# Optimization experiments

Hardware: AMD Instinct MI355X
Metric: run time of the kernel (lower is better)

Reference implementation:

```python
import jax, jax.numpy as jnp
import numpy as np

B, S = 256, 512
NQ = 1000           # n_skills
MEM, DK, DV, FC = 20, 50, 200, 50  # memory_size, key dim, value dim, final fc dim


def _kaiming(key, shape, fan_in):
    return jax.random.normal(key, shape) * np.float32(np.sqrt(2.0 / fan_in))


def setup_inputs() -> dict:
    key = jax.random.key(0)
    ks = jax.random.split(key, 12)
    q_data = jax.random.randint(ks[0], (B, S), 0, NQ + 1)
    qa_data = jax.random.randint(ks[1], (B, S), 0, 2 * NQ + 1)
    u = jax.random.uniform(ks[2], (B * S,))
    # target: -1 = masked/padding, else binary label (matches target.ge(0) masking)
    target = jnp.where(u < 0.1, -1.0, (u > 0.55).astype(jnp.float32))
    q_embed_w = _kaiming(ks[3], (NQ + 1, DK), DK)
    qa_embed_w = _kaiming(ks[4], (2 * NQ + 1, DV), DV)
    memory_key = _kaiming(ks[5], (MEM, DK), DK)
    init_memory_value = _kaiming(ks[6], (MEM, DV), DV)
    erase_w = _kaiming(ks[7], (DV, DV), DV)
    erase_b = jnp.zeros((DV,), jnp.float32)
    add_w = _kaiming(ks[8], (DV, DV), DV)
    add_b = jnp.zeros((DV,), jnp.float32)
    read_w = _kaiming(ks[9], (DV + FC, FC), DV + FC)
    read_b = jnp.zeros((FC,), jnp.float32)
    pred_w = _kaiming(ks[10], (FC, 1), FC)
    pred_b = jnp.zeros((1,), jnp.float32)
    return dict(q_data=q_data, qa_data=qa_data, target=target,
                q_embed_w=q_embed_w, qa_embed_w=qa_embed_w,
                memory_key=memory_key, init_memory_value=init_memory_value,
                erase_w=erase_w, erase_b=erase_b, add_w=add_w, add_b=add_b,
                read_w=read_w, read_b=read_b, pred_w=pred_w, pred_b=pred_b)


def reference(q_data, qa_data, target, q_embed_w, qa_embed_w, memory_key,
              init_memory_value, erase_w, erase_b, add_w, add_b,
              read_w, read_b, pred_w, pred_b):
    b = q_data.shape[0]
    q_e = q_embed_w[q_data]     # [B,S,DK]
    qa_e = qa_embed_w[qa_data]  # [B,S,DV]
    Mv0 = jnp.broadcast_to(init_memory_value, (b, MEM, DV))

    def step(Mv, xs):
        q_t, qa_t = xs                                        # [B,DK], [B,DV]
        corr = jax.nn.softmax(q_t @ memory_key.T, axis=1)     # [B,MEM] addressing
        read = jnp.einsum('bm,bmd->bd', corr, Mv)             # weighted read
        erase = jax.nn.sigmoid(qa_t @ erase_w + erase_b)      # [B,DV]
        add = jnp.tanh(qa_t @ add_w + add_b)                  # [B,DV]
        w = corr[:, :, None]                                  # [B,MEM,1]
        Mv = Mv * (1.0 - w * erase[:, None, :]) + w * add[:, None, :]
        return Mv, read

    _, reads = jax.lax.scan(step, Mv0, (q_e.transpose(1, 0, 2), qa_e.transpose(1, 0, 2)))
    reads = reads.transpose(1, 0, 2)                          # [B,S,DV]
    x = jnp.concatenate([reads, q_e], axis=-1)                # [B,S,DV+FC]
    h = jnp.tanh(x @ read_w + read_b)                         # [B,S,FC]
    logits = (h @ pred_w + pred_b).reshape(-1)                # [B*S]
    mask = target >= 0.0
    t = jnp.where(mask, target, 0.0)
    # numerically-stable BCE-with-logits, masked mean
    bce = jnp.maximum(logits, 0.0) - logits * t + jnp.log1p(jnp.exp(-jnp.abs(logits)))
    loss = jnp.sum(jnp.where(mask, bce, 0.0)) / jnp.maximum(mask.sum(), 1)
    return loss, jax.nn.sigmoid(logits)
```

## Files before the change

### kernel.cpp

```cpp
#include <hip/hip_runtime.h>
#include <math.h>

#define B_   256
#define S_   512
#define NQ_  1000
#define MEM_ 20
#define DK_  50
#define DV_  200
#define FC_  50
#define RPB  4
#define CHK  16
#define CLEN (S_/CHK)
#define NKS  7
#define XS_STRIDE 232
#define NB_EA    ((2*NQ_+1+RPB-1)/RPB)
#define NB_CORR  4
#define NB_WPACK 7
#define NB_HQ    251
#define PREP_BLOCKS (NB_EA+NB_CORR+NB_WPACK+NB_HQ)
#define MM_BLOCKS (B_*CHK)
#define SCANA_BLOCKS (B_*(CHK-1))

typedef __attribute__((ext_vector_type(8))) short bf16x8_t;
typedef __attribute__((ext_vector_type(4))) float f32x4_t;
typedef __attribute__((ext_vector_type(2))) float f32x2_t;

static __device__ __forceinline__ f32x2_t pkfma(f32x2_t a, f32x2_t b, f32x2_t c){
  return __builtin_elementwise_fma(a, b, c);
}

static __device__ __forceinline__ unsigned short f2bf(float f){
  unsigned u = __float_as_uint(f);
  unsigned r = u + 0x7fffu + ((u >> 16) & 1u);
  return (unsigned short)(r >> 16);
}
static __device__ __forceinline__ float bf2f_lo(unsigned v){ return __uint_as_float(v << 16); }
static __device__ __forceinline__ float bf2f_hi(unsigned v){ return __uint_as_float(v & 0xffff0000u); }
static __device__ __forceinline__ float ftanh(float x){
  float e = __expf(2.f*x);
  return 1.f - 2.f*__builtin_amdgcn_rcpf(e+1.f);
}
static __device__ __forceinline__ float fsigm(float x){
  return __builtin_amdgcn_rcpf(1.f+__expf(-x));
}

__global__ __launch_bounds__(256) void k_prep(
    const float* __restrict__ qaw,
    const float* __restrict__ ew, const float* __restrict__ eb,
    const float* __restrict__ aw, const float* __restrict__ ab,
    float2* __restrict__ eaTab,
    const float* __restrict__ qw, const float* __restrict__ mk,
    float* __restrict__ corrTab,
    const float* __restrict__ rw, const float* __restrict__ rb,
    const float* __restrict__ pw,
    unsigned short* __restrict__ WpFrag, float* __restrict__ pwPad,
    float* __restrict__ hq){
  __shared__ float qa[RPB*DV_];
  int blk = blockIdx.x;
  if(blk < NB_EA){
    int row0 = blk*RPB;
    for(int i=threadIdx.x; i<RPB*DV_; i+=256){
      int r = i/DV_, cc = i - r*DV_;
      int row = row0 + r;
      qa[i] = (row <= 2*NQ_) ? qaw[row*DV_+cc] : 0.f;
    }
    __syncthreads();
    int d = threadIdx.x;
    if(d >= DV_) return;
    float accE[RPB], accA[RPB];
    #pragma unroll
    for(int r=0;r<RPB;++r){ accE[r] = eb[d]; accA[r] = ab[d]; }
    float we0 = ew[d], wa0 = aw[d];
    for(int j=0;j<DV_;++j){
      int jn = (j+1 < DV_) ? j+1 : j;
      float we1 = ew[jn*DV_+d];
      float wa1 = aw[jn*DV_+d];
      #pragma unroll
      for(int r=0;r<RPB;++r){
        float x = qa[r*DV_+j];
        accE[r] = fmaf(x, we0, accE[r]);
        accA[r] = fmaf(x, wa0, accA[r]);
      }
      we0 = we1; wa0 = wa1;
    }
    #pragma unroll
    for(int r=0;r<RPB;++r){
      int row = row0 + r;
      if(row <= 2*NQ_)
        eaTab[(size_t)row*DV_+d] = make_float2(fsigm(accE[r]), ftanh(accA[r]));
    }
  } else if(blk < NB_EA+NB_CORR){
    int q = (blk-NB_EA)*256 + threadIdx.x;
    if(q > NQ_) return;
    float qv[DK_];
    #pragma unroll
    for(int j=0;j<DK_;++j) qv[j] = qw[q*DK_+j];
    float s[MEM_]; float mx = -1e30f;
    #pragma unroll
    for(int m=0;m<MEM_;++m){
      float acc = 0.f;
      #pragma unroll
      for(int j=0;j<DK_;++j) acc = fmaf(qv[j], mk[m*DK_+j], acc);
      s[m] = acc; mx = fmaxf(mx, acc);
    }
    float sum = 0.f;
    #pragma unroll
    for(int m=0;m<MEM_;++m){ s[m] = __expf(s[m]-mx); sum += s[m]; }
    float inv = __builtin_amdgcn_rcpf(sum);
    #pragma unroll
    for(int m=0;m<MEM_;++m) corrTab[q*MEM_+m] = s[m]*inv;
  } else if(blk < NB_EA+NB_CORR+NB_WPACK){
    int ks = blk - (NB_EA+NB_CORR);
    int nt = threadIdx.x >> 6;
    int lane = threadIdx.x & 63;
    int quad = lane >> 4, col = lane & 15;
    int n = nt*16 + col;
    unsigned short tmp[8];
    #pragma unroll
    for(int j=0;j<8;++j){
      int k = ks*32 + quad*8 + j;
      tmp[j] = (k < DV_ && n < FC_) ? f2bf(rw[k*FC_+n]) : (unsigned short)0;
    }
    uint4* dst = reinterpret_cast<uint4*>(WpFrag + ((size_t)(ks*4+nt)*64 + lane)*8);
    *dst = *reinterpret_cast<const uint4*>(tmp);
    if(ks == 0 && threadIdx.x < 64)
      pwPad[threadIdx.x] = (threadIdx.x < FC_) ? pw[threadIdx.x] : 0.f;
  } else {
    int idx = (blk-(NB_EA+NB_CORR+NB_WPACK))*256 + threadIdx.x;
    int q = idx >> 6, n = idx & 63;
    if(q > NQ_) return;
    float v = 0.f;
    if(n < FC_){
      float acc = rb[n];
      #pragma unroll
      for(int j=0;j<DK_;++j)
        acc = fmaf(qw[q*DK_+j], rw[(DV_+j)*FC_+n], acc);
      v = acc;
    }
    hq[q*64+n] = v;
  }
}

__global__ __launch_bounds__(256,8) void k_scanA(const int* __restrict__ qd,
    const int* __restrict__ qad,
    const float4* __restrict__ corr4,
    const float2* __restrict__ eaTab,
    unsigned* __restrict__ ABu){
  const int blk = blockIdx.x;
  const int b = blk / (CHK-1), c = blk % (CHK-1);
  const int d = threadIdx.x;
  const int dc = (d < DV_) ? d : DV_-1;
  const bool act = (d < DV_);
  const int* __restrict__ qp  = qd  + b*S_ + c*CLEN;
  const int* __restrict__ qap = qad + b*S_ + c*CLEN;

  f32x2_t A2[MEM_/2], B2[MEM_/2];
  #pragma unroll
  for(int i=0;i<MEM_/2;++i){ A2[i] = (f32x2_t){1.f,1.f}; B2[i] = (f32x2_t){0.f,0.f}; }

  int q2  = qp[1];
  int qa2 = qap[1];
  int q1s = __builtin_amdgcn_readfirstlane(qp[0]);
  int qa1 = qap[0];
  const float4* cb0 = corr4 + q1s*5;
  float4 c0 = cb0[0], c1 = cb0[1], c2 = cb0[2], c3 = cb0[3], c4 = cb0[4];
  float2 ea = eaTab[(size_t)qa1*DV_ + dc];

  #pragma unroll 2
  for(int t=0;t<CLEN;++t){
    int t2 = (t+2 < CLEN) ? t+2 : CLEN-1;
    int q3 = qp[t2], qa3 = qap[t2];
    int qs = __builtin_amdgcn_readfirstlane(q2);
    const float4* cb = corr4 + qs*5;
    float4 n0 = cb[0], n1 = cb[1], n2 = cb[2], n3 = cb[3], n4 = cb[4];
    float2 ean = eaTab[(size_t)qa2*DV_ + dc];

    const f32x2_t e2 = {ea.x, ea.x}, a2 = {ea.y, ea.y}, one2 = {1.f, 1.f};
    #define UPDA(cx, cy, i) { \
      f32x2_t cp = {cx, cy}; \
      f32x2_t al = pkfma(-cp, e2, one2); \
      f32x2_t be = cp*a2; \
      A2[i] = A2[i]*al; \
      B2[i] = pkfma(al, B2[i], be); }
    UPDA(c0.x, c0.y, 0)  UPDA(c0.z, c0.w, 1)
    UPDA(c1.x, c1.y, 2)  UPDA(c1.z, c1.w, 3)
    UPDA(c2.x, c2.y, 4)  UPDA(c2.z, c2.w, 5)
    UPDA(c3.x, c3.y, 6)  UPDA(c3.z, c3.w, 7)
    UPDA(c4.x, c4.y, 8)  UPDA(c4.z, c4.w, 9)
    #undef UPDA

    c0=n0; c1=n1; c2=n2; c3=n3; c4=n4; ea=ean;
    q2=q3; qa2=qa3;
  }
  if(act){
    unsigned* base = ABu + ((size_t)(b*(CHK-1) + c)*MEM_)*DV_ + d;
    #pragma unroll
    for(int i=0;i<MEM_/2;++i){
      base[(size_t)(2*i)*DV_]   = (unsigned)f2bf(A2[i][0]) | ((unsigned)f2bf(B2[i][0]) << 16);
      base[(size_t)(2*i+1)*DV_] = (unsigned)f2bf(A2[i][1]) | ((unsigned)f2bf(B2[i][1]) << 16);
    }
  }
}

__global__ __launch_bounds__(256) void k_prefix(const float* __restrict__ mv0,
    const unsigned* __restrict__ ABu, unsigned short* __restrict__ Mv0s){
  int i = blockIdx.x*256 + threadIdx.x;
  if(i >= B_*MEM_*DV_) return;
  int d = i % DV_;
  int m = (i / DV_) % MEM_;
  int b = i / (DV_*MEM_);
  unsigned abv[CHK-1];
  #pragma unroll
  for(int c=0;c<CHK-1;++c)
    abv[c] = ABu[((size_t)(b*(CHK-1) + c)*MEM_ + m)*DV_ + d];
  float Mv = mv0[m*DV_+d];
  #pragma unroll
  for(int c=0;c<CHK;++c){
    Mv0s[((size_t)(b*CHK + c)*MEM_ + m)*DV_ + d] = f2bf(Mv);
    if(c < CHK-1) Mv = fmaf(bf2f_lo(abv[c]), Mv, bf2f_hi(abv[c]));
  }
}

__global__ __launch_bounds__(256,8) void k_scan_mm(const int* __restrict__ qd,
    const int* __restrict__ qad,
    const float4* __restrict__ corr4,
    const float2* __restrict__ eaTab,
    const unsigned short* __restrict__ Mv0s,
    const unsigned short* __restrict__ WpFrag,
    const float* __restrict__ hq,
    const float* __restrict__ pwPad, const float* __restrict__ pb,
    const float* __restrict__ target,
    float* __restrict__ out, float2* __restrict__ partials){
  __shared__ unsigned short Xs[CLEN*XS_STRIDE];
  __shared__ float sred[2][2][16];
  __shared__ float sbce[4];

  const int blk = blockIdx.x;
  const int b = blk >> 4, c = blk & (CHK-1);
  const int d = threadIdx.x;
  const int dc = (d < DV_) ? d : DV_-1;
  const bool act = (d < DV_);
  const bool padw = (d < 224);
  const int* __restrict__ qp  = qd  + b*S_ + c*CLEN;
  const int* __restrict__ qap = qad + b*S_ + c*CLEN;

  f32x2_t Mv2[MEM_/2];
  {
    const unsigned short* base = Mv0s + ((size_t)(b*CHK + c)*MEM_)*DV_ + dc;
    #pragma unroll
    for(int i=0;i<MEM_/2;++i)
      Mv2[i] = (f32x2_t){ bf2f_lo((unsigned)base[(size_t)(2*i)*DV_]),
                          bf2f_lo((unsigned)base[(size_t)(2*i+1)*DV_]) };
  }

  int q2  = qp[1];
  int qa2 = qap[1];
  int q1s = __builtin_amdgcn_readfirstlane(qp[0]);
  int qa1 = qap[0];
  const float4* cbi = corr4 + q1s*5;
  float4 c0 = cbi[0], c1 = cbi[1], c2 = cbi[2], c3 = cbi[3], c4 = cbi[4];
  float2 ea = eaTab[(size_t)qa1*DV_ + dc];

  #pragma unroll 2
  for(int t=0;t<CLEN;++t){
    int t2 = (t+2 < CLEN) ? t+2 : CLEN-1;
    int q3 = qp[t2], qa3 = qap[t2];
    int qs = __builtin_amdgcn_readfirstlane(q2);
    const float4* cb = corr4 + qs*5;
    float4 n0 = cb[0], n1 = cb[1], n2 = cb[2], n3 = cb[3], n4 = cb[4];
    float2 ean = eaTab[(size_t)qa2*DV_ + dc];

    const f32x2_t e2 = {ea.x, ea.x}, a2 = {ea.y, ea.y};
    f32x2_t rd2 = {0.f, 0.f};
    #define UPD2(cx, cy, i) { \
      f32x2_t cp = {cx, cy}; \
      rd2 = pkfma(cp, Mv2[i], rd2); \
      Mv2[i] = pkfma(cp, pkfma(-Mv2[i], e2, a2), Mv2[i]); }
    UPD2(c0.x, c0.y, 0)  UPD2(c0.z, c0.w, 1)
    UPD2(c1.x, c1.y, 2)  UPD2(c1.z, c1.w, 3)
    UPD2(c2.x, c2.y, 4)  UPD2(c2.z, c2.w, 5)
    UPD2(c3.x, c3.y, 6)  UPD2(c3.z, c3.w, 7)
    UPD2(c4.x, c4.y, 8)  UPD2(c4.z, c4.w, 9)
    #undef UPD2

    if(padw) Xs[t*XS_STRIDE + d] = act ? f2bf(rd2[0]+rd2[1]) : (unsigned short)0;

    c0=n0; c1=n1; c2=n2; c3=n3; c4=n4; ea=ean;
    q2=q3; qa2=qa3;
  }
  __syncthreads();

  const int wave = threadIdx.x >> 6;
  const int lane = threadIdx.x & 63;
  const int col  = lane & 15, quad = lane >> 4;
  const int rt   = wave & 1;
  const int nh   = wave >> 1;
  const int mbase = rt*16;

  f32x4_t acc[2];
  acc[0] = (f32x4_t){0.f,0.f,0.f,0.f};
  acc[1] = (f32x4_t){0.f,0.f,0.f,0.f};

  #pragma unroll
  for(int ks=0;ks<NKS;++ks){
    bf16x8_t a = *reinterpret_cast<const bf16x8_t*>(Xs + (mbase+col)*XS_STRIDE + quad*8 + ks*32);
    #pragma unroll
    for(int j=0;j<2;++j){
      int nt = nh*2 + j;
      bf16x8_t bfr = *reinterpret_cast<const bf16x8_t*>(WpFrag + ((size_t)(ks*4+nt)*64 + lane)*8);
      acc[j] = __builtin_amdgcn_mfma_f32_16x16x32_bf16(a, bfr, acc[j], 0, 0, 0);
    }
  }

  float part[4];
  #pragma unroll
  for(int reg=0;reg<4;++reg){
    int mloc = mbase + quad*4 + reg;
    int q = qp[mloc];
    float s = 0.f;
    #pragma unroll
    for(int j=0;j<2;++j){
      int n = (nh*2+j)*16 + col;
      float h = acc[j][reg] + hq[q*64 + n];
      s = fmaf(pwPad[n], ftanh(h), s);
    }
    part[reg] = s;
  }
  #pragma unroll
  for(int off=1; off<16; off<<=1){
    #pragma unroll
    for(int reg=0;reg<4;++reg) part[reg] += __shfl_xor(part[reg], off, 64);
  }
  if(col == 0){
    #pragma unroll
    for(int reg=0;reg<4;++reg) sred[rt][nh][quad*4+reg] = part[reg];
  }
  __syncthreads();

  float bce = 0.f, cnt = 0.f;
  if(nh == 0 && col == 0){
    float pbv = pb[0];
    #pragma unroll
    for(int reg=0;reg<4;++reg){
      int idx = quad*4 + reg;
      int mloc = mbase + idx;
      int row = b*S_ + c*CLEN + mloc;
      float logit = sred[rt][0][idx] + sred[rt][1][idx] + pbv;
      out[1+row] = fsigm(logit);
      float t = target[row];
      if(t >= 0.f){
        cnt += 1.f;
        bce += fmaxf(logit,0.f) - logit*t + log1pf(__expf(-fabsf(logit)));
      }
    }
  }
  bce += __shfl_xor(bce, 16, 64); cnt += __shfl_xor(cnt, 16, 64);
  bce += __shfl_xor(bce, 32, 64); cnt += __shfl_xor(cnt, 32, 64);
  if(lane == 0 && nh == 0){ sbce[wave] = bce; sbce[2+wave] = cnt; }
  __syncthreads();
  if(threadIdx.x == 0)
    partials[blk] = make_float2(sbce[0]+sbce[1], sbce[2]+sbce[3]);
}

__global__ __launch_bounds__(256) void k_fin(const float2* __restrict__ partials,
                                             float* __restrict__ out){
  float bce = 0.f, cnt = 0.f;
  for(int i=threadIdx.x; i<MM_BLOCKS; i+=256){
    float2 p = partials[i];
    bce += p.x; cnt += p.y;
  }
  #pragma unroll
  for(int off=32; off>0; off>>=1){
    bce += __shfl_down(bce, off, 64);
    cnt += __shfl_down(cnt, off, 64);
  }
  __shared__ float sb[4], sc[4];
  int w = threadIdx.x >> 6;
  if((threadIdx.x & 63) == 0){ sb[w] = bce; sc[w] = cnt; }
  __syncthreads();
  if(threadIdx.x == 0){
    float Bt = sb[0]+sb[1]+sb[2]+sb[3];
    float Ct = sc[0]+sc[1]+sc[2]+sc[3];
    out[0] = Bt / fmaxf(Ct, 1.f);
  }
}

extern "C" void kernel_launch(void* const* d_in, const int* in_sizes, int n_in,
                              void* d_out, int out_size, void* d_ws, size_t ws_size,
                              hipStream_t stream){
  const int*   qd     = (const int*)d_in[0];
  const int*   qad    = (const int*)d_in[1];
  const float* target = (const float*)d_in[2];
  const float* qw     = (const float*)d_in[3];
  const float* qaw    = (const float*)d_in[4];
  const float* mk     = (const float*)d_in[5];
  const float* mv0    = (const float*)d_in[6];
  const float* ew     = (const float*)d_in[7];
  const float* eb     = (const float*)d_in[8];
  const float* aw     = (const float*)d_in[9];
  const float* ab     = (const float*)d_in[10];
  const float* rw     = (const float*)d_in[11];
  const float* rb     = (const float*)d_in[12];
  const float* pw     = (const float*)d_in[13];
  const float* pb     = (const float*)d_in[14];
  float* out = (float*)d_out;

  char* ws = (char*)d_ws;
  size_t off = 0;
  float2* partials = (float2*)(ws + off);            off += (size_t)MM_BLOCKS*8;
  float* corrTab  = (float*)(ws + off);              off += (((size_t)(NQ_+1)*MEM_*4 + 255)/256)*256;
  float2* eaTab   = (float2*)(ws + off);             off += (((size_t)(2*NQ_+1)*DV_*8 + 255)/256)*256;
  unsigned* ABu   = (unsigned*)(ws + off);           off += (size_t)SCANA_BLOCKS*MEM_*DV_*4;
  unsigned short* Mv0s = (unsigned short*)(ws + off); off += (size_t)MM_BLOCKS*MEM_*DV_*2;
  unsigned short* WpFrag = (unsigned short*)(ws + off); off += ((size_t)NKS*4*64*8*2 + 255)/256*256;
  float* pwPad    = (float*)(ws + off);              off += 256;
  float* hq       = (float*)(ws + off);              off += (size_t)(NQ_+1)*64*4;

  k_prep<<<dim3(PREP_BLOCKS), dim3(256), 0, stream>>>(qaw, ew, eb, aw, ab, eaTab,
                                                      qw, mk, corrTab,
                                                      rw, rb, pw, WpFrag, pwPad, hq);
  k_scanA<<<dim3(SCANA_BLOCKS), dim3(256), 0, stream>>>(qd, qad, (const float4*)corrTab, (const float2*)eaTab, ABu);
  k_prefix<<<dim3((B_*MEM_*DV_+255)/256), dim3(256), 0, stream>>>(mv0, ABu, Mv0s);
  k_scan_mm<<<dim3(MM_BLOCKS), dim3(256), 0, stream>>>(qd, qad, (const float4*)corrTab, (const float2*)eaTab,
                                                       Mv0s, WpFrag, hq, pwPad, pb, target, out, partials);
  k_fin<<<dim3(1), dim3(256), 0, stream>>>(partials, out);
}
```

Measured before the change: 226.9 us.

## Halve scan chunk count and process each chunk in two 32-step sub-tiles

Reduces the number of sequence chunks per batch row from 16 to 8, so each scan block walks 64 steps in two 32-step sub-tiles, running the MFMA readout and BCE after each sub-tile from a reused shared buffer. This halves the chunk-prefix work and the Mv0 state traffic (fewer chunk starting states to compute and load), and halves the block count. In exchange each block's sequential scan is twice as long, there are fewer blocks to hide latency, and an extra barrier pair is added per sub-tile. It relies on the prep kernels using CHK consistently for the chunk-start states.

```diff
diff --git a/kernel.cpp b/kernel.cpp
--- a/kernel.cpp
+++ b/kernel.cpp
@@ -9,8 +9,9 @@
 #define DV_  200
 #define FC_  50
 #define RPB  4
-#define CHK  16
+#define CHK  8
 #define CLEN (S_/CHK)
+#define SUB  32
 #define NKS  7
 #define XS_STRIDE 232
 #define NB_EA    ((2*NQ_+1+RPB-1)/RPB)
@@ -231,12 +232,12 @@
     const float* __restrict__ pwPad, const float* __restrict__ pb,
     const float* __restrict__ target,
     float* __restrict__ out, float2* __restrict__ partials){
-  __shared__ unsigned short Xs[CLEN*XS_STRIDE];
+  __shared__ unsigned short Xs[SUB*XS_STRIDE];
   __shared__ float sred[2][2][16];
   __shared__ float sbce[4];
 
   const int blk = blockIdx.x;
-  const int b = blk >> 4, c = blk & (CHK-1);
+  const int b = blk >> 3, c = blk & (CHK-1);
   const int d = threadIdx.x;
   const int dc = (d < DV_) ? d : DV_-1;
   const bool act = (d < DV_);
@@ -261,35 +262,6 @@
   float4 c0 = cbi[0], c1 = cbi[1], c2 = cbi[2], c3 = cbi[3], c4 = cbi[4];
   float2 ea = eaTab[(size_t)qa1*DV_ + dc];
 
-  #pragma unroll 2
-  for(int t=0;t<CLEN;++t){
-    int t2 = (t+2 < CLEN) ? t+2 : CLEN-1;
-    int q3 = qp[t2], qa3 = qap[t2];
-    int qs = __builtin_amdgcn_readfirstlane(q2);
-    const float4* cb = corr4 + qs*5;
-    float4 n0 = cb[0], n1 = cb[1], n2 = cb[2], n3 = cb[3], n4 = cb[4];
-    float2 ean = eaTab[(size_t)qa2*DV_ + dc];
-
-    const f32x2_t e2 = {ea.x, ea.x}, a2 = {ea.y, ea.y};
-    f32x2_t rd2 = {0.f, 0.f};
-    #define UPD2(cx, cy, i) { \
-      f32x2_t cp = {cx, cy}; \
-      rd2 = pkfma(cp, Mv2[i], rd2); \
-      Mv2[i] = pkfma(cp, pkfma(-Mv2[i], e2, a2), Mv2[i]); }
-    UPD2(c0.x, c0.y, 0)  UPD2(c0.z, c0.w, 1)
-    UPD2(c1.x, c1.y, 2)  UPD2(c1.z, c1.w, 3)
-    UPD2(c2.x, c2.y, 4)  UPD2(c2.z, c2.w, 5)
-    UPD2(c3.x, c3.y, 6)  UPD2(c3.z, c3.w, 7)
-    UPD2(c4.x, c4.y, 8)  UPD2(c4.z, c4.w, 9)
-    #undef UPD2
-
-    if(padw) Xs[t*XS_STRIDE + d] = act ? f2bf(rd2[0]+rd2[1]) : (unsigned short)0;
-
-    c0=n0; c1=n1; c2=n2; c3=n3; c4=n4; ea=ean;
-    q2=q3; qa2=qa3;
-  }
-  __syncthreads();
-
   const int wave = threadIdx.x >> 6;
   const int lane = threadIdx.x & 63;
   const int col  = lane & 15, quad = lane >> 4;
@@ -297,63 +269,99 @@
   const int nh   = wave >> 1;
   const int mbase = rt*16;
 
-  f32x4_t acc[2];
-  acc[0] = (f32x4_t){0.f,0.f,0.f,0.f};
-  acc[1] = (f32x4_t){0.f,0.f,0.f,0.f};
+  float bceAcc = 0.f, cntAcc = 0.f;
+  const float pbv = pb[0];
 
   #pragma unroll
-  for(int ks=0;ks<NKS;++ks){
-    bf16x8_t a = *reinterpret_cast<const bf16x8_t*>(Xs + (mbase+col)*XS_STRIDE + quad*8 + ks*32);
-    #pragma unroll
-    for(int j=0;j<2;++j){
-      int nt = nh*2 + j;
-      bf16x8_t bfr = *reinterpret_cast<const bf16x8_t*>(WpFrag + ((size_t)(ks*4+nt)*64 + lane)*8);
-      acc[j] = __builtin_amdgcn_mfma_f32_16x16x32_bf16(a, bfr, acc[j], 0, 0, 0);
-    }
-  }
-
-  float part[4];
-  #pragma unroll
-  for(int reg=0;reg<4;++reg){
-    int mloc = mbase + quad*4 + reg;
-    int q = qp[mloc];
-    float s = 0.f;
-    #pragma unroll
-    for(int j=0;j<2;++j){
-      int n = (nh*2+j)*16 + col;
-      float h = acc[j][reg] + hq[q*64 + n];
-      s = fmaf(pwPad[n], ftanh(h), s);
-    }
-    part[reg] = s;
-  }
-  #pragma unroll
-  for(int off=1; off<16; off<<=1){
-    #pragma unroll
-    for(int reg=0;reg<4;++reg) part[reg] += __shfl_xor(part[reg], off, 64);
-  }
-  if(col == 0){
-    #pragma unroll
-    for(int reg=0;reg<4;++reg) sred[rt][nh][quad*4+reg] = part[reg];
-  }
-  __syncthreads();
-
-  float bce = 0.f, cnt = 0.f;
-  if(nh == 0 && col == 0){
-    float pbv = pb[0];
+  for(int sub=0; sub<2; ++sub){
+    #pragma unroll 2
+    for(int i=0;i<SUB;++i){
+      int t = sub*SUB + i;
+      int t2 = (t+2 < CLEN) ? t+2 : CLEN-1;
+      int q3 = qp[t2], qa3 = qap[t2];
+      int qs = __builtin_amdgcn_readfirstlane(q2);
+      const float4* cb = corr4 + qs*5;
+      float4 n0 = cb[0], n1 = cb[1], n2 = cb[2], n3 = cb[3], n4 = cb[4];
+      float2 ean = eaTab[(size_t)qa2*DV_ + dc];
+
+      const f32x2_t e2 = {ea.x, ea.x}, a2 = {ea.y, ea.y};
+      f32x2_t rd2 = {0.f, 0.f};
+      #define UPD2(cx, cy, i2) { \
+        f32x2_t cp = {cx, cy}; \
+        rd2 = pkfma(cp, Mv2[i2], rd2); \
+        Mv2[i2] = pkfma(cp, pkfma(-Mv2[i2], e2, a2), Mv2[i2]); }
+      UPD2(c0.x, c0.y, 0)  UPD2(c0.z, c0.w, 1)
+      UPD2(c1.x, c1.y, 2)  UPD2(c1.z, c1.w, 3)
+      UPD2(c2.x, c2.y, 4)  UPD2(c2.z, c2.w, 5)
+      UPD2(c3.x, c3.y, 6)  UPD2(c3.z, c3.w, 7)
+      UPD2(c4.x, c4.y, 8)  UPD2(c4.z, c4.w, 9)
+      #undef UPD2
+
+      if(padw) Xs[i*XS_STRIDE + d] = act ? f2bf(rd2[0]+rd2[1]) : (unsigned short)0;
+
+      c0=n0; c1=n1; c2=n2; c3=n3; c4=n4; ea=ean;
+      q2=q3; qa2=qa3;
+    }
+    __syncthreads();
+
+    f32x4_t acc[2];
+    acc[0] = (f32x4_t){0.f,0.f,0.f,0.f};
+    acc[1] = (f32x4_t){0.f,0.f,0.f,0.f};
+
+    #pragma unroll
+    for(int ks=0;ks<NKS;++ks){
+      bf16x8_t a = *reinterpret_cast<const bf16x8_t*>(Xs + (mbase+col)*XS_STRIDE + quad*8 + ks*32);
+      #pragma unroll
+      for(int j=0;j<2;++j){
+        int nt = nh*2 + j;
+        bf16x8_t bfr = *reinterpret_cast<const bf16x8_t*>(WpFrag + ((size_t)(ks*4+nt)*64 + lane)*8);
+        acc[j] = __builtin_amdgcn_mfma_f32_16x16x32_bf16(a, bfr, acc[j], 0, 0, 0);
+      }
+    }
+
+    float part[4];
     #pragma unroll
     for(int reg=0;reg<4;++reg){
-      int idx = quad*4 + reg;
-      int mloc = mbase + idx;
-      int row = b*S_ + c*CLEN + mloc;
-      float logit = sred[rt][0][idx] + sred[rt][1][idx] + pbv;
-      out[1+row] = fsigm(logit);
-      float t = target[row];
-      if(t >= 0.f){
-        cnt += 1.f;
-        bce += fmaxf(logit,0.f) - logit*t + log1pf(__expf(-fabsf(logit)));
+      int mloc = mbase + quad*4 + reg;
+      int q = qp[sub*SUB + mloc];
+      float s = 0.f;
+      #pragma unroll
+      for(int j=0;j<2;++j){
+        int n = (nh*2+j)*16 + col;
+        float h = acc[j][reg] + hq[q*64 + n];
+        s = fmaf(pwPad[n], ftanh(h), s);
       }
-    }
-  }
+      part[reg] = s;
+    }
+    #pragma unroll
+    for(int off=1; off<16; off<<=1){
+      #pragma unroll
+      for(int reg=0;reg<4;++reg) part[reg] += __shfl_xor(part[reg], off, 64);
+    }
+    if(col == 0){
+      #pragma unroll
+      for(int reg=0;reg<4;++reg) sred[rt][nh][quad*4+reg] = part[reg];
+    }
+    __syncthreads();
+
+    if(nh == 0 && col == 0){
+      #pragma unroll
+      for(int reg=0;reg<4;++reg){
+        int idx = quad*4 + reg;
+        int mloc = mbase + idx;
+        int row = b*S_ + c*CLEN + sub*SUB + mloc;
+        float logit = sred[rt][0][idx] + sred[rt][1][idx] + pbv;
+        out[1+row] = fsigm(logit);
+        float t = target[row];
+        if(t >= 0.f){
+          cntAcc += 1.f;
+          bceAcc += fmaxf(logit,0.f) - logit*t + log1pf(__expf(-fabsf(logit)));
+        }
+      }
+    }
+  }
+
+  float bce = bceAcc, cnt = cntAcc;
   bce += __shfl_xor(bce, 16, 64); cnt += __shfl_xor(cnt, 16, 64);
   bce += __shfl_xor(bce, 32, 64); cnt += __shfl_xor(cnt, 32, 64);
   if(lane == 0 && nh == 0){ sbce[wave] = bce; sbce[2+wave] = cnt; }
```

New measurement: 227.6 us. About the same (+0.3%).

## Move weight packing into scanA launch, deepen eaTab prefetch, skip chunk-0 state store

Applied to the files above, without the earlier changes.

Moves the WpFrag/pwPad/hq preparation blocks out of the prep kernel into extra blocks of the scanA launch, so the prep kernel on the critical path is shorter. Deepens the erase/add table prefetch in both scan loops to two steps ahead, with index lookahead of four. Chunk 0 now reads the initial memory directly instead of a stored bf16 copy, so the prefix kernel skips that write. The hq gather indices are loaded early in scan_mm. This costs extra registers, which may reduce occupancy.

```diff
diff --git a/kernel.cpp b/kernel.cpp
--- a/kernel.cpp
+++ b/kernel.cpp
@@ -17,9 +17,10 @@
 #define NB_CORR  4
 #define NB_WPACK 7
 #define NB_HQ    251
-#define PREP_BLOCKS (NB_EA+NB_CORR+NB_WPACK+NB_HQ)
+#define PREP1_BLOCKS (NB_EA+NB_CORR)
 #define MM_BLOCKS (B_*CHK)
 #define SCANA_BLOCKS (B_*(CHK-1))
+#define SCANA_TOTAL (SCANA_BLOCKS+NB_WPACK+NB_HQ)
 
 typedef __attribute__((ext_vector_type(8))) short bf16x8_t;
 typedef __attribute__((ext_vector_type(4))) float f32x4_t;
@@ -44,17 +45,13 @@
   return __builtin_amdgcn_rcpf(1.f+__expf(-x));
 }
 
-__global__ __launch_bounds__(256) void k_prep(
+__global__ __launch_bounds__(256) void k_prep1(
     const float* __restrict__ qaw,
     const float* __restrict__ ew, const float* __restrict__ eb,
     const float* __restrict__ aw, const float* __restrict__ ab,
     float2* __restrict__ eaTab,
     const float* __restrict__ qw, const float* __restrict__ mk,
-    float* __restrict__ corrTab,
-    const float* __restrict__ rw, const float* __restrict__ rb,
-    const float* __restrict__ pw,
-    unsigned short* __restrict__ WpFrag, float* __restrict__ pwPad,
-    float* __restrict__ hq){
+    float* __restrict__ corrTab){
   __shared__ float qa[RPB*DV_];
   int blk = blockIdx.x;
   if(blk < NB_EA){
@@ -89,7 +86,7 @@
       if(row <= 2*NQ_)
         eaTab[(size_t)row*DV_+d] = make_float2(fsigm(accE[r]), ftanh(accA[r]));
     }
-  } else if(blk < NB_EA+NB_CORR){
+  } else {
     int q = (blk-NB_EA)*256 + threadIdx.x;
     if(q > NQ_) return;
     float qv[DK_];
@@ -109,35 +106,6 @@
     float inv = __builtin_amdgcn_rcpf(sum);
     #pragma unroll
     for(int m=0;m<MEM_;++m) corrTab[q*MEM_+m] = s[m]*inv;
-  } else if(blk < NB_EA+NB_CORR+NB_WPACK){
-    int ks = blk - (NB_EA+NB_CORR);
-    int nt = threadIdx.x >> 6;
-    int lane = threadIdx.x & 63;
-    int quad = lane >> 4, col = lane & 15;
-    int n = nt*16 + col;
-    unsigned short tmp[8];
-    #pragma unroll
-    for(int j=0;j<8;++j){
-      int k = ks*32 + quad*8 + j;
-      tmp[j] = (k < DV_ && n < FC_) ? f2bf(rw[k*FC_+n]) : (unsigned short)0;
-    }
-    uint4* dst = reinterpret_cast<uint4*>(WpFrag + ((size_t)(ks*4+nt)*64 + lane)*8);
-    *dst = *reinterpret_cast<const uint4*>(tmp);
-    if(ks == 0 && threadIdx.x < 64)
-      pwPad[threadIdx.x] = (threadIdx.x < FC_) ? pw[threadIdx.x] : 0.f;
-  } else {
-    int idx = (blk-(NB_EA+NB_CORR+NB_WPACK))*256 + threadIdx.x;
-    int q = idx >> 6, n = idx & 63;
-    if(q > NQ_) return;
-    float v = 0.f;
-    if(n < FC_){
-      float acc = rb[n];
-      #pragma unroll
-      for(int j=0;j<DK_;++j)
-        acc = fmaf(qw[q*DK_+j], rw[(DV_+j)*FC_+n], acc);
-      v = acc;
-    }
-    hq[q*64+n] = v;
   }
 }
 
@@ -145,8 +113,48 @@
     const int* __restrict__ qad,
     const float4* __restrict__ corr4,
     const float2* __restrict__ eaTab,
-    unsigned* __restrict__ ABu){
+    unsigned* __restrict__ ABu,
+    const float* __restrict__ qw,
+    const float* __restrict__ rw, const float* __restrict__ rb,
+    const float* __restrict__ pw,
+    unsigned short* __restrict__ WpFrag, float* __restrict__ pwPad,
+    float* __restrict__ hq){
   const int blk = blockIdx.x;
+  if(blk >= SCANA_BLOCKS){
+    int xblk = blk - SCANA_BLOCKS;
+    if(xblk < NB_WPACK){
+      int ks = xblk;
+      int nt = threadIdx.x >> 6;
+      int lane = threadIdx.x & 63;
+      int quad = lane >> 4, col = lane & 15;
+      int n = nt*16 + col;
+      unsigned short tmp[8];
+      #pragma unroll
+      for(int j=0;j<8;++j){
+        int k = ks*32 + quad*8 + j;
+        tmp[j] = (k < DV_ && n < FC_) ? f2bf(rw[k*FC_+n]) : (unsigned short)0;
+      }
+      uint4* dst = reinterpret_cast<uint4*>(WpFrag + ((size_t)(ks*4+nt)*64 + lane)*8);
+      *dst = *reinterpret_cast<const uint4*>(tmp);
+      if(ks == 0 && threadIdx.x < 64)
+        pwPad[threadIdx.x] = (threadIdx.x < FC_) ? pw[threadIdx.x] : 0.f;
+    } else {
+      int idx = (xblk-NB_WPACK)*256 + threadIdx.x;
+      int q = idx >> 6, n = idx & 63;
+      if(q > NQ_) return;
+      float v = 0.f;
+      if(n < FC_){
+        float acc = rb[n];
+        #pragma unroll
+        for(int j=0;j<DK_;++j)
+          acc = fmaf(qw[q*DK_+j], rw[(DV_+j)*FC_+n], acc);
+        v = acc;
+      }
+      hq[q*64+n] = v;
+    }
+    return;
+  }
+
   const int b = blk / (CHK-1), c = blk % (CHK-1);
   const int d = threadIdx.x;
   const int dc = (d < DV_) ? d : DV_-1;
@@ -158,22 +166,25 @@
   #pragma unroll
   for(int i=0;i<MEM_/2;++i){ A2[i] = (f32x2_t){1.f,1.f}; B2[i] = (f32x2_t){0.f,0.f}; }
 
-  int q2  = qp[1];
-  int qa2 = qap[1];
-  int q1s = __builtin_amdgcn_readfirstlane(qp[0]);
-  int qa1 = qap[0];
+  int q2   = qp[1];
+  int qaT2 = qap[2];
+  int qaT3 = qap[3];
+  int q1s  = __builtin_amdgcn_readfirstlane(qp[0]);
   const float4* cb0 = corr4 + q1s*5;
   float4 c0 = cb0[0], c1 = cb0[1], c2 = cb0[2], c3 = cb0[3], c4 = cb0[4];
-  float2 ea = eaTab[(size_t)qa1*DV_ + dc];
+  float2 ea  = eaTab[(size_t)qap[0]*DV_ + dc];
+  float2 ean = eaTab[(size_t)qap[1]*DV_ + dc];
 
   #pragma unroll 2
   for(int t=0;t<CLEN;++t){
     int t2 = (t+2 < CLEN) ? t+2 : CLEN-1;
-    int q3 = qp[t2], qa3 = qap[t2];
+    int t4 = (t+4 < CLEN) ? t+4 : CLEN-1;
+    int q3 = qp[t2];
+    int qaN = qap[t4];
     int qs = __builtin_amdgcn_readfirstlane(q2);
     const float4* cb = corr4 + qs*5;
     float4 n0 = cb[0], n1 = cb[1], n2 = cb[2], n3 = cb[3], n4 = cb[4];
-    float2 ean = eaTab[(size_t)qa2*DV_ + dc];
+    float2 eann = eaTab[(size_t)qaT2*DV_ + dc];
 
     const f32x2_t e2 = {ea.x, ea.x}, a2 = {ea.y, ea.y}, one2 = {1.f, 1.f};
     #define UPDA(cx, cy, i) { \
@@ -189,8 +200,9 @@
     UPDA(c4.x, c4.y, 8)  UPDA(c4.z, c4.w, 9)
     #undef UPDA
 
-    c0=n0; c1=n1; c2=n2; c3=n3; c4=n4; ea=ean;
-    q2=q3; qa2=qa3;
+    c0=n0; c1=n1; c2=n2; c3=n3; c4=n4;
+    ea=ean; ean=eann;
+    q2=q3; qaT2=qaT3; qaT3=qaN;
   }
   if(act){
     unsigned* base = ABu + ((size_t)(b*(CHK-1) + c)*MEM_)*DV_ + d;
@@ -215,9 +227,10 @@
     abv[c] = ABu[((size_t)(b*(CHK-1) + c)*MEM_ + m)*DV_ + d];
   float Mv = mv0[m*DV_+d];
   #pragma unroll
-  for(int c=0;c<CHK;++c){
+  for(int c=1;c<CHK;++c){
+    unsigned v = abv[c-1];
+    Mv = fmaf(bf2f_lo(v), Mv, bf2f_hi(v));
     Mv0s[((size_t)(b*CHK + c)*MEM_ + m)*DV_ + d] = f2bf(Mv);
-    if(c < CHK-1) Mv = fmaf(bf2f_lo(abv[c]), Mv, bf2f_hi(abv[c]));
   }
 }
 
@@ -225,6 +238,7 @@
     const int* __restrict__ qad,
     const float4* __restrict__ corr4,
     const float2* __restrict__ eaTab,
+    const float* __restrict__ mv0,
     const unsigned short* __restrict__ Mv0s,
     const unsigned short* __restrict__ WpFrag,
     const float* __restrict__ hq,
@@ -244,8 +258,23 @@
   const int* __restrict__ qp  = qd  + b*S_ + c*CLEN;
   const int* __restrict__ qap = qad + b*S_ + c*CLEN;
 
+  const int wave = threadIdx.x >> 6;
+  const int lane = threadIdx.x & 63;
+  const int col  = lane & 15, quad = lane >> 4;
+  const int rt   = wave & 1;
+  const int nh   = wave >> 1;
+  const int mbase = rt*16;
+
+  int qpre[4];
+  #pragma unroll
+  for(int reg=0;reg<4;++reg) qpre[reg] = qp[mbase + quad*4 + reg];
+
   f32x2_t Mv2[MEM_/2];
-  {
+  if(c == 0){
+    #pragma unroll
+    for(int i=0;i<MEM_/2;++i)
+      Mv2[i] = (f32x2_t){ mv0[(2*i)*DV_+dc], mv0[(2*i+1)*DV_+dc] };
+  } else {
     const unsigned short* base = Mv0s + ((size_t)(b*CHK + c)*MEM_)*DV_ + dc;
     #pragma unroll
     for(int i=0;i<MEM_/2;++i)
@@ -253,22 +282,25 @@
                           bf2f_lo((unsigned)base[(size_t)(2*i+1)*DV_]) };
   }
 
-  int q2  = qp[1];
-  int qa2 = qap[1];
-  int q1s = __builtin_amdgcn_readfirstlane(qp[0]);
-  int qa1 = qap[0];
+  int q2   = qp[1];
+  int qaT2 = qap[2];
+  int qaT3 = qap[3];
+  int q1s  = __builtin_amdgcn_readfirstlane(qp[0]);
   const float4* cbi = corr4 + q1s*5;
   float4 c0 = cbi[0], c1 = cbi[1], c2 = cbi[2], c3 = cbi[3], c4 = cbi[4];
-  float2 ea = eaTab[(size_t)qa1*DV_ + dc];
+  float2 ea  = eaTab[(size_t)qap[0]*DV_ + dc];
+  float2 ean = eaTab[(size_t)qap[1]*DV_ + dc];
 
   #pragma unroll 2
   for(int t=0;t<CLEN;++t){
     int t2 = (t+2 < CLEN) ? t+2 : CLEN-1;
-    int q3 = qp[t2], qa3 = qap[t2];
+    int t4 = (t+4 < CLEN) ? t+4 : CLEN-1;
+    int q3 = qp[t2];
+    int qaN = qap[t4];
     int qs = __builtin_amdgcn_readfirstlane(q2);
     const float4* cb = corr4 + qs*5;
     float4 n0 = cb[0], n1 = cb[1], n2 = cb[2], n3 = cb[3], n4 = cb[4];
-    float2 ean = eaTab[(size_t)qa2*DV_ + dc];
+    float2 eann = eaTab[(size_t)qaT2*DV_ + dc];
 
     const f32x2_t e2 = {ea.x, ea.x}, a2 = {ea.y, ea.y};
     f32x2_t rd2 = {0.f, 0.f};
@@ -285,17 +317,18 @@
 
     if(padw) Xs[t*XS_STRIDE + d] = act ? f2bf(rd2[0]+rd2[1]) : (unsigned short)0;
 
-    c0=n0; c1=n1; c2=n2; c3=n3; c4=n4; ea=ean;
-    q2=q3; qa2=qa3;
+    c0=n0; c1=n1; c2=n2; c3=n3; c4=n4;
+    ea=ean; ean=eann;
+    q2=q3; qaT2=qaT3; qaT3=qaN;
   }
   __syncthreads();
 
-  const int wave = threadIdx.x >> 6;
-  const int lane = threadIdx.x & 63;
-  const int col  = lane & 15, quad = lane >> 4;
-  const int rt   = wave & 1;
-  const int nh   = wave >> 1;
-  const int mbase = rt*16;
+  float hqv[4][2];
+  #pragma unroll
+  for(int reg=0;reg<4;++reg)
+    #pragma unroll
+    for(int j=0;j<2;++j)
+      hqv[reg][j] = hq[qpre[reg]*64 + (nh*2+j)*16 + col];
 
   f32x4_t acc[2];
   acc[0] = (f32x4_t){0.f,0.f,0.f,0.f};
@@ -315,13 +348,11 @@
   float part[4];
   #pragma unroll
   for(int reg=0;reg<4;++reg){
-    int mloc = mbase + quad*4 + reg;
-    int q = qp[mloc];
     float s = 0.f;
     #pragma unroll
     for(int j=0;j<2;++j){
       int n = (nh*2+j)*16 + col;
-      float h = acc[j][reg] + hq[q*64 + n];
+      float h = acc[j][reg] + hqv[reg][j];
       s = fmaf(pwPad[n], ftanh(h), s);
     }
     part[reg] = s;
@@ -416,12 +447,12 @@
   float* pwPad    = (float*)(ws + off);              off += 256;
   float* hq       = (float*)(ws + off);              off += (size_t)(NQ_+1)*64*4;
 
-  k_prep<<<dim3(PREP_BLOCKS), dim3(256), 0, stream>>>(qaw, ew, eb, aw, ab, eaTab,
-                                                      qw, mk, corrTab,
-                                                      rw, rb, pw, WpFrag, pwPad, hq);
-  k_scanA<<<dim3(SCANA_BLOCKS), dim3(256), 0, stream>>>(qd, qad, (const float4*)corrTab, (const float2*)eaTab, ABu);
+  k_prep1<<<dim3(PREP1_BLOCKS), dim3(256), 0, stream>>>(qaw, ew, eb, aw, ab, eaTab,
+                                                        qw, mk, corrTab);
+  k_scanA<<<dim3(SCANA_TOTAL), dim3(256), 0, stream>>>(qd, qad, (const float4*)corrTab, (const float2*)eaTab,
+                                                       ABu, qw, rw, rb, pw, WpFrag, pwPad, hq);
   k_prefix<<<dim3((B_*MEM_*DV_+255)/256), dim3(256), 0, stream>>>(mv0, ABu, Mv0s);
   k_scan_mm<<<dim3(MM_BLOCKS), dim3(256), 0, stream>>>(qd, qad, (const float4*)corrTab, (const float2*)eaTab,
-                                                       Mv0s, WpFrag, hq, pwPad, pb, target, out, partials);
+                                                       mv0, Mv0s, WpFrag, hq, pwPad, pb, target, out, partials);
   k_fin<<<dim3(1), dim3(256), 0, stream>>>(partials, out);
 }
```

After: 228.1 us. No clear change (+0.5%).
